# Performance work log

Measured on AMD Instinct MI355X. Metric: run time of the kernel, lower is better.

The kernel has to match this reference:

```python
import jax, jax.numpy as jnp
import numpy as np

S, D, H, L, FF = 4096, 128, 4, 3, 1024
DH = D // H
LN_EPS = 1e-5


def _layernorm(x, g, b):
    m = jnp.mean(x, axis=-1, keepdims=True)
    v = jnp.mean((x - m) ** 2, axis=-1, keepdims=True)
    return (x - m) * jax.lax.rsqrt(v + LN_EPS) * g + b


def setup_inputs() -> dict:
    key = jax.random.key(0)
    ks = jax.random.split(key, 16)
    w = lambda k, shp, s=0.05: jax.random.normal(k, shp, dtype=jnp.float32) * s
    return {
        "src": jax.random.normal(ks[0], (S, 1, D), dtype=jnp.float32),
        # per-layer transformer params, stacked on leading L axis
        "Wqkv": w(ks[1], (L, 3 * D, D)),
        "bqkv": jnp.zeros((L, 3 * D), jnp.float32),
        "Wo": w(ks[2], (L, D, D)),
        "bo": jnp.zeros((L, D), jnp.float32),
        "ln1_g": jnp.ones((L, D), jnp.float32),
        "ln1_b": jnp.zeros((L, D), jnp.float32),
        "W1": w(ks[3], (L, FF, D)),
        "b1": jnp.zeros((L, FF), jnp.float32),
        "W2": w(ks[4], (L, D, FF)),
        "b2": jnp.zeros((L, D), jnp.float32),
        "ln2_g": jnp.ones((L, D), jnp.float32),
        "ln2_b": jnp.zeros((L, D), jnp.float32),
        "fc1_W": w(ks[5], (D, D)),
        "fc1_b": jnp.zeros((D,), jnp.float32),
        "fc2_W": w(ks[6], (D, D)),
        "fc2_b": jnp.zeros((D,), jnp.float32),
    }


def reference(src, Wqkv, bqkv, Wo, bo, ln1_g, ln1_b, W1, b1, W2, b2,
              ln2_g, ln2_b, fc1_W, fc1_b, fc2_W, fc2_b):
    x = src[:, 0, :]  # [S, D] (batch=1, squeezed as in the torch module)
    scale = 1.0 / np.sqrt(DH).astype(np.float32)
    for l in range(L):  # small fixed layer count
        # --- self-attention (post-norm, as in torch TransformerEncoderLayer, eval mode) ---
        qkv = x @ Wqkv[l].T + bqkv[l]                      # [S, 3D]
        q, k, v = jnp.split(qkv, 3, axis=-1)
        q = q.reshape(S, H, DH)
        k = k.reshape(S, H, DH)
        v = v.reshape(S, H, DH)
        att = jax.nn.softmax(jnp.einsum('shd,thd->hst', q, k) * scale, axis=-1)
        o = jnp.einsum('hst,thd->shd', att, v).reshape(S, D)
        o = o @ Wo[l].T + bo[l]
        x = _layernorm(x + o, ln1_g[l], ln1_b[l])
        # --- feed-forward ---
        f = jax.nn.relu(x @ W1[l].T + b1[l]) @ W2[l].T + b2[l]
        x = _layernorm(x + f, ln2_g[l], ln2_b[l])
    # head
    x = jax.nn.relu(x @ fc1_W.T + fc1_b)
    x = x @ fc2_W.T + fc2_b
    # pairwise cosine similarity, clamped at min 1e-6 (vectorized form of pCosineSim)
    xn = x / jnp.linalg.norm(x, axis=1, keepdims=True)
    return jnp.maximum(xn @ xn.T, 1e-6)
```

## Files before the change

### kernel.cpp

```cpp
#include <hip/hip_runtime.h>
#include <math.h>

#define S 4096
#define QK_SCALE 0.17677669529663687f
#define LOG2E    1.44269504088896f
#define SPLIT 8
#define KS (S / SPLIT)

typedef _Float16 f16x8 __attribute__((ext_vector_type(8)));
typedef _Float16 f16x4 __attribute__((ext_vector_type(4)));
typedef _Float16 f16x2 __attribute__((ext_vector_type(2)));
typedef float f32x4 __attribute__((ext_vector_type(4)));

template<int R>
__device__ __forceinline__ void stageT(_Float16 (*dst)[136], const _Float16* __restrict__ src,
                                       int ld, int row0, int col0, int tid) {
    int r = tid >> 4, cb = (tid & 15) * 8;
#pragma unroll
    for (int v = 0; v < R / 16; v++)
        *(f16x8*)&dst[v * 16 + r][cb] =
            *(const f16x8*)(src + (size_t)(row0 + v * 16 + r) * ld + col0 + cb);
}

__device__ __forceinline__ void stageA_f16(_Float16 (*dst)[72], const _Float16* src,
                                           int ld, int row0, int col0, int tid) {
    int sr = tid >> 1, sc = (tid & 1) * 32;
    const _Float16* p = src + (size_t)(row0 + sr) * ld + col0 + sc;
#pragma unroll
    for (int v = 0; v < 4; v++)
        *(f16x8*)&dst[sr][sc + v * 8] = *(const f16x8*)(p + v * 8);
}

__device__ __forceinline__ void mfma_tiles(_Float16 (*Ah)[72], _Float16 (*Bh)[72],
                                           int wrow, int wcol, int lc, int lr,
                                           f32x4 acc[4][4]) {
#pragma unroll
    for (int ks = 0; ks < 2; ks++) {
        f16x8 afr[4], bfr[4];
#pragma unroll
        for (int t = 0; t < 4; t++) {
            afr[t] = *(const f16x8*)&Ah[wrow + t * 16 + lc][ks * 32 + lr * 8];
            bfr[t] = *(const f16x8*)&Bh[wcol + t * 16 + lc][ks * 32 + lr * 8];
        }
#pragma unroll
        for (int i = 0; i < 4; i++)
#pragma unroll
            for (int j = 0; j < 4; j++)
                acc[i][j] = __builtin_amdgcn_mfma_f32_16x16x32_f16(
                    afr[i], bfr[j], acc[i][j], 0, 0, 0);
    }
}

__global__ __launch_bounds__(256) void cvt_weights(const float* __restrict__ q,
                                                   const float* __restrict__ wo,
                                                   const float* __restrict__ w1,
                                                   const float* __restrict__ w2,
                                                   const float* __restrict__ f1,
                                                   const float* __restrict__ f2,
                                                   _Float16* __restrict__ dst)
{
    int bb = blockIdx.x;
    const float* src; size_t dof; int lb;
    if (bb < 144)      { src = q;  dof = 0;      lb = bb; }
    else if (bb < 192) { src = wo; dof = 147456; lb = bb - 144; }
    else if (bb < 576) { src = w1; dof = 196608; lb = bb - 192; }
    else if (bb < 960) { src = w2; dof = 589824; lb = bb - 576; }
    else if (bb < 976) { src = f1; dof = 983040; lb = bb - 960; }
    else               { src = f2; dof = 999424; lb = bb - 976; }
    int i = lb * 1024 + threadIdx.x * 4;
    float4 v = *(const float4*)(src + i);
    f16x4 h = {(_Float16)v.x, (_Float16)v.y, (_Float16)v.z, (_Float16)v.w};
    *(f16x4*)(dst + dof + i) = h;
}

__global__ __launch_bounds__(256) void copy_x(const float* __restrict__ a,
                                              float* __restrict__ x,
                                              _Float16* __restrict__ xh) {
    int i = blockIdx.x * 256 + threadIdx.x;
    float4 v = ((const float4*)a)[i];
    ((float4*)x)[i] = v;
    f16x4 h = {(_Float16)v.x, (_Float16)v.y, (_Float16)v.z, (_Float16)v.w};
    ((f16x4*)xh)[i] = h;
}

__global__ __launch_bounds__(256) void gemm_qkv(const _Float16* __restrict__ xh,
                                                const _Float16* __restrict__ Wh,
                                                const float* __restrict__ bias,
                                                _Float16* __restrict__ qh,
                                                _Float16* __restrict__ kh,
                                                _Float16* __restrict__ vt)
{
    __shared__ _Float16 Ah[32][136], Bh[128][136];
    int tid = threadIdx.x, w = tid >> 6, l = tid & 63, lc = l & 15, lr = l >> 4;
    int wr = w >> 1, wc = w & 1;
    int m0 = blockIdx.x * 32, by = blockIdx.y;

    stageT<32>(Ah, xh, 128, m0, 0, tid);
    stageT<128>(Bh, Wh, 128, by * 128, 0, tid);
    __syncthreads();

    f32x4 acc[4];
#pragma unroll
    for (int j = 0; j < 4; j++) acc[j] = {0.f, 0.f, 0.f, 0.f};
#pragma unroll
    for (int ks = 0; ks < 4; ks++) {
        f16x8 af = *(const f16x8*)&Ah[wr * 16 + lc][ks * 32 + lr * 8];
#pragma unroll
        for (int j = 0; j < 4; j++) {
            f16x8 bf = *(const f16x8*)&Bh[wc * 64 + j * 16 + lc][ks * 32 + lr * 8];
            acc[j] = __builtin_amdgcn_mfma_f32_16x16x32_f16(af, bf, acc[j], 0, 0, 0);
        }
    }

    int mb = m0 + wr * 16 + lr * 4;
#pragma unroll
    for (int j = 0; j < 4; j++) {
        int n = wc * 64 + j * 16 + lc;
        float bb = bias[by * 128 + n];
        if (by == 0) {
#pragma unroll
            for (int r = 0; r < 4; r++)
                qh[(size_t)(mb + r) * 128 + n] =
                    (_Float16)((acc[j][r] + bb) * (QK_SCALE * LOG2E));
        } else if (by == 1) {
            int hh = n >> 5, d = n & 31;
#pragma unroll
            for (int r = 0; r < 4; r++)
                kh[((size_t)hh * S + mb + r) * 32 + d] = (_Float16)(acc[j][r] + bb);
        } else {
            f16x4 pk;
#pragma unroll
            for (int r = 0; r < 4; r++) pk[r] = (_Float16)(acc[j][r] + bb);
            *(f16x4*)&vt[(size_t)n * S + mb] = pk;
        }
    }
}

__global__ __launch_bounds__(256) void attn_mfma(const _Float16* __restrict__ qh,
                                                 const _Float16* __restrict__ kh,
                                                 const _Float16* __restrict__ vt,
                                                 _Float16* __restrict__ part,
                                                 float* __restrict__ mll)
{
    __shared__ _Float16 Ks[64][48];
    __shared__ _Float16 Vt[32][72];
    __shared__ _Float16 Ps[4][16][72];
    int h = blockIdx.y, q0 = blockIdx.x * 64, z = blockIdx.z;
    int tid = threadIdx.x;
    int w = tid >> 6, l = tid & 63;
    int lc = l & 15, lr = l >> 4;

    f16x8 qf = *(const f16x8*)&qh[(size_t)(q0 + w * 16 + lc) * 128 + h * 32 + lr * 8];

    f32x4 o0 = {0.f, 0.f, 0.f, 0.f}, o1 = {0.f, 0.f, 0.f, 0.f};
    float lp[4] = {0.f, 0.f, 0.f, 0.f};

    const _Float16* khh = kh + (size_t)h * S * 32;
    const _Float16* vth = vt + (size_t)h * 32 * S;

    for (int k0 = z * KS; k0 < z * KS + KS; k0 += 64) {
        __syncthreads();
        {
            int row = tid >> 2, dg = (tid & 3) * 8;
            *(f16x8*)&Ks[row][dg] = *(const f16x8*)&khh[(size_t)(k0 + row) * 32 + dg];
            int dim = tid >> 3, kg = (tid & 7) * 8;
            *(f16x8*)&Vt[dim][kg] = *(const f16x8*)&vth[(size_t)dim * S + k0 + kg];
        }
        __syncthreads();

        f32x4 st[4];
#pragma unroll
        for (int t = 0; t < 4; t++) {
            f16x8 kf = *(const f16x8*)&Ks[t * 16 + lc][lr * 8];
            f32x4 zz = {0.f, 0.f, 0.f, 0.f};
            st[t] = __builtin_amdgcn_mfma_f32_16x16x32_f16(qf, kf, zz, 0, 0, 0);
        }

#pragma unroll
        for (int i = 0; i < 4; i++) {
            float p0 = exp2f(st[0][i]), p1 = exp2f(st[1][i]);
            float p2 = exp2f(st[2][i]), p3 = exp2f(st[3][i]);
            lp[i] += (p0 + p1) + (p2 + p3);
            Ps[w][lr * 4 + i][lc]      = (_Float16)p0;
            Ps[w][lr * 4 + i][16 + lc] = (_Float16)p1;
            Ps[w][lr * 4 + i][32 + lc] = (_Float16)p2;
            Ps[w][lr * 4 + i][48 + lc] = (_Float16)p3;
        }
        asm volatile("s_waitcnt lgkmcnt(0)" ::: "memory");
#pragma unroll
        for (int ch = 0; ch < 2; ch++) {
            f16x8 pf = *(const f16x8*)&Ps[w][lc][ch * 32 + lr * 8];
            f16x8 v0 = *(const f16x8*)&Vt[lc][ch * 32 + lr * 8];
            f16x8 v1 = *(const f16x8*)&Vt[16 + lc][ch * 32 + lr * 8];
            o0 = __builtin_amdgcn_mfma_f32_16x16x32_f16(pf, v0, o0, 0, 0, 0);
            o1 = __builtin_amdgcn_mfma_f32_16x16x32_f16(pf, v1, o1, 0, 0, 0);
        }
    }

#pragma unroll
    for (int i = 0; i < 4; i++) {
#pragma unroll
        for (int off = 1; off < 16; off <<= 1) lp[i] += __shfl_xor(lp[i], off);
    }

    _Float16* pz = part + (size_t)z * 524288;
#pragma unroll
    for (int i = 0; i < 4; i++) {
        int q = q0 + w * 16 + lr * 4 + i;
        pz[(size_t)q * 128 + h * 32 + lc]      = (_Float16)o0[i];
        pz[(size_t)q * 128 + h * 32 + 16 + lc] = (_Float16)o1[i];
        if (lc == 0) mll[((size_t)z * 4 + h) * 4096 + q] = lp[i];
    }
}

__global__ __launch_bounds__(256) void wo_ln_merge(const _Float16* __restrict__ part,
                                                   const float* __restrict__ mll,
                                                   const _Float16* __restrict__ Wh,
                                                   const float* __restrict__ bias,
                                                   float* __restrict__ x,
                                                   _Float16* __restrict__ xh,
                                                   const float* __restrict__ g,
                                                   const float* __restrict__ b)
{
    __shared__ _Float16 Ah[16][136], Bh[128][136];
    __shared__ float Red[16][4][2];
    int tid = threadIdx.x, w = tid >> 6, l = tid & 63, lc = l & 15, lr = l >> 4;
    int m0 = blockIdx.x * 16;

    {
        int row = tid >> 4, col0 = (tid & 15) * 8;
        int q = m0 + row, hh = col0 >> 5;
        float lsum = 0.f;
#pragma unroll
        for (int s = 0; s < SPLIT; s++) lsum += mll[((size_t)s * 4 + hh) * 4096 + q];
        float am[8];
#pragma unroll
        for (int e = 0; e < 8; e++) am[e] = 0.f;
#pragma unroll
        for (int s = 0; s < SPLIT; s++) {
            f16x8 t = *(const f16x8*)&part[(size_t)s * 524288 + (size_t)q * 128 + col0];
#pragma unroll
            for (int e = 0; e < 8; e++) am[e] += (float)t[e];
        }
        float inv = 1.f / lsum;
        f16x8 hv;
#pragma unroll
        for (int e = 0; e < 8; e++) hv[e] = (_Float16)(am[e] * inv);
        *(f16x8*)&Ah[row][col0] = hv;
    }
    stageT<128>(Bh, Wh, 128, 0, 0, tid);
    __syncthreads();

    f32x4 acc[2];
#pragma unroll
    for (int j = 0; j < 2; j++) acc[j] = {0.f, 0.f, 0.f, 0.f};
#pragma unroll
    for (int ks = 0; ks < 4; ks++) {
        f16x8 af = *(const f16x8*)&Ah[lc][ks * 32 + lr * 8];
#pragma unroll
        for (int j = 0; j < 2; j++) {
            f16x8 bf = *(const f16x8*)&Bh[w * 32 + j * 16 + lc][ks * 32 + lr * 8];
            acc[j] = __builtin_amdgcn_mfma_f32_16x16x32_f16(af, bf, acc[j], 0, 0, 0);
        }
    }

#pragma unroll
    for (int j = 0; j < 2; j++) {
        int n = w * 32 + j * 16 + lc;
        float bb = bias[n];
#pragma unroll
        for (int r = 0; r < 4; r++)
            acc[j][r] += bb + x[(size_t)(m0 + lr * 4 + r) * 128 + n];
    }
#pragma unroll
    for (int r = 0; r < 4; r++) {
        float s1 = acc[0][r] + acc[1][r];
        float s2 = acc[0][r] * acc[0][r] + acc[1][r] * acc[1][r];
#pragma unroll
        for (int off = 1; off < 16; off <<= 1) {
            s1 += __shfl_xor(s1, off);
            s2 += __shfl_xor(s2, off);
        }
        if (lc == 0) { Red[lr * 4 + r][w][0] = s1; Red[lr * 4 + r][w][1] = s2; }
    }
    __syncthreads();
#pragma unroll
    for (int r = 0; r < 4; r++) {
        int rl = lr * 4 + r;
        float S1 = (Red[rl][0][0] + Red[rl][1][0]) + (Red[rl][2][0] + Red[rl][3][0]);
        float S2 = (Red[rl][0][1] + Red[rl][1][1]) + (Red[rl][2][1] + Red[rl][3][1]);
        float mean = S1 * (1.0f / 128.0f);
        float var = S2 * (1.0f / 128.0f) - mean * mean;
        float inv = rsqrtf(var + 1e-5f);
        int m = m0 + rl;
#pragma unroll
        for (int j = 0; j < 2; j++) {
            int n = w * 32 + j * 16 + lc;
            float o = (acc[j][r] - mean) * inv * g[n] + b[n];
            x[(size_t)m * 128 + n] = o;
            xh[(size_t)m * 128 + n] = (_Float16)o;
        }
    }
}

__global__ __launch_bounds__(256) void ffn_pair(const _Float16* __restrict__ xh,
                                                const _Float16* __restrict__ W1h,
                                                const float* __restrict__ b1,
                                                const _Float16* __restrict__ W2h,
                                                _Float16* __restrict__ wpart)
{
    __shared__ _Float16 Ah[64][136], Bh[128][136];
    int tid = threadIdx.x, w = tid >> 6, l = tid & 63, lc = l & 15, lr = l >> 4;
    int wr = w >> 1, wc = w & 1;
    int m0 = blockIdx.x * 64, c = blockIdx.y;

    stageT<64>(Ah, xh, 128, m0, 0, tid);
    stageT<128>(Bh, W1h, 128, c * 128, 0, tid);
    __syncthreads();

    f32x4 acc[2][4];
#pragma unroll
    for (int i = 0; i < 2; i++)
#pragma unroll
        for (int j = 0; j < 4; j++) acc[i][j] = {0.f, 0.f, 0.f, 0.f};
#pragma unroll
    for (int ks = 0; ks < 4; ks++) {
        f16x8 af0 = *(const f16x8*)&Ah[wr * 32 + lc][ks * 32 + lr * 8];
        f16x8 af1 = *(const f16x8*)&Ah[wr * 32 + 16 + lc][ks * 32 + lr * 8];
#pragma unroll
        for (int j = 0; j < 4; j++) {
            f16x8 bf = *(const f16x8*)&Bh[wc * 64 + j * 16 + lc][ks * 32 + lr * 8];
            acc[0][j] = __builtin_amdgcn_mfma_f32_16x16x32_f16(af0, bf, acc[0][j], 0, 0, 0);
            acc[1][j] = __builtin_amdgcn_mfma_f32_16x16x32_f16(af1, bf, acc[1][j], 0, 0, 0);
        }
    }
    __syncthreads();

#pragma unroll
    for (int i = 0; i < 2; i++)
#pragma unroll
        for (int j = 0; j < 4; j++) {
            int n = wc * 64 + j * 16 + lc;
            float bb = b1[c * 128 + n];
#pragma unroll
            for (int r = 0; r < 4; r++)
                Ah[wr * 32 + i * 16 + lr * 4 + r][n] =
                    (_Float16)fmaxf(acc[i][j][r] + bb, 0.f);
        }
    stageT<128>(Bh, W2h, 1024, 0, c * 128, tid);
    __syncthreads();

    f32x4 oacc[2][4];
#pragma unroll
    for (int i = 0; i < 2; i++)
#pragma unroll
        for (int j = 0; j < 4; j++) oacc[i][j] = {0.f, 0.f, 0.f, 0.f};
#pragma unroll
    for (int ks = 0; ks < 4; ks++) {
        f16x8 af0 = *(const f16x8*)&Ah[wr * 32 + lc][ks * 32 + lr * 8];
        f16x8 af1 = *(const f16x8*)&Ah[wr * 32 + 16 + lc][ks * 32 + lr * 8];
#pragma unroll
        for (int j = 0; j < 4; j++) {
            f16x8 bf = *(const f16x8*)&Bh[wc * 64 + j * 16 + lc][ks * 32 + lr * 8];
            oacc[0][j] = __builtin_amdgcn_mfma_f32_16x16x32_f16(af0, bf, oacc[0][j], 0, 0, 0);
            oacc[1][j] = __builtin_amdgcn_mfma_f32_16x16x32_f16(af1, bf, oacc[1][j], 0, 0, 0);
        }
    }

    _Float16* pz = wpart + (size_t)c * 524288;
#pragma unroll
    for (int i = 0; i < 2; i++) {
        int mb = m0 + wr * 32 + i * 16 + lr * 4;
#pragma unroll
        for (int j = 0; j < 4; j++) {
            int n = wc * 64 + j * 16 + lc;
#pragma unroll
            for (int r = 0; r < 4; r++)
                pz[(size_t)(mb + r) * 128 + n] = (_Float16)oacc[i][j][r];
        }
    }
}

__global__ __launch_bounds__(256) void reduce8_ln(const _Float16* __restrict__ part,
                                                  const float* __restrict__ bias,
                                                  float* __restrict__ x,
                                                  _Float16* __restrict__ xh,
                                                  const float* __restrict__ g,
                                                  const float* __restrict__ b)
{
    int row  = blockIdx.x * 4 + (threadIdx.x >> 6);
    int lane = threadIdx.x & 63;
    size_t base = (size_t)row * 128;
    int c = lane * 2;
    float a0 = 0.f, a1 = 0.f;
#pragma unroll
    for (int s = 0; s < 8; s++) {
        f16x2 p = *(const f16x2*)&part[(size_t)s * 524288 + base + c];
        a0 += (float)p[0]; a1 += (float)p[1];
    }
    float2 bv = *(const float2*)&bias[c];
    float2 xv = *(const float2*)&x[base + c];
    a0 += bv.x + xv.x; a1 += bv.y + xv.y;
    float s = a0 + a1;
#pragma unroll
    for (int off = 32; off; off >>= 1) s += __shfl_xor(s, off);
    float mean = s * (1.0f / 128.0f);
    float d0 = a0 - mean, d1 = a1 - mean;
    float v = d0 * d0 + d1 * d1;
#pragma unroll
    for (int off = 32; off; off >>= 1) v += __shfl_xor(v, off);
    float inv = rsqrtf(v * (1.0f / 128.0f) + 1e-5f);
    float2 gv = *(const float2*)&g[c];
    float2 bb = *(const float2*)&b[c];
    float o0 = d0 * inv * gv.x + bb.x, o1 = d1 * inv * gv.y + bb.y;
    float2 r; r.x = o0; r.y = o1;
    *(float2*)&x[base + c] = r;
    f16x2 rh = {(_Float16)o0, (_Float16)o1};
    *(f16x2*)&xh[base + c] = rh;
}

__global__ __launch_bounds__(256) void fc_fused(const _Float16* __restrict__ xh,
                                                const _Float16* __restrict__ W1h,
                                                const float* __restrict__ b1f,
                                                const _Float16* __restrict__ W2h,
                                                const float* __restrict__ b2f,
                                                _Float16* __restrict__ aoh)
{
    __shared__ _Float16 Ah[16][136], Bh[128][136];
    __shared__ float Red[16][4];
    int tid = threadIdx.x, w = tid >> 6, l = tid & 63, lc = l & 15, lr = l >> 4;
    int m0 = blockIdx.x * 16;

    stageT<16>(Ah, xh, 128, m0, 0, tid);
    stageT<128>(Bh, W1h, 128, 0, 0, tid);
    __syncthreads();

    f32x4 acc[2];
#pragma unroll
    for (int j = 0; j < 2; j++) acc[j] = {0.f, 0.f, 0.f, 0.f};
#pragma unroll
    for (int ks = 0; ks < 4; ks++) {
        f16x8 af = *(const f16x8*)&Ah[lc][ks * 32 + lr * 8];
#pragma unroll
        for (int j = 0; j < 2; j++) {
            f16x8 bf = *(const f16x8*)&Bh[w * 32 + j * 16 + lc][ks * 32 + lr * 8];
            acc[j] = __builtin_amdgcn_mfma_f32_16x16x32_f16(af, bf, acc[j], 0, 0, 0);
        }
    }
    __syncthreads();
#pragma unroll
    for (int j = 0; j < 2; j++) {
        int n = w * 32 + j * 16 + lc;
        float bb = b1f[n];
#pragma unroll
        for (int r = 0; r < 4; r++)
            Ah[lr * 4 + r][n] = (_Float16)fmaxf(acc[j][r] + bb, 0.f);
    }
    stageT<128>(Bh, W2h, 128, 0, 0, tid);
    __syncthreads();

    f32x4 o[2];
#pragma unroll
    for (int j = 0; j < 2; j++) o[j] = {0.f, 0.f, 0.f, 0.f};
#pragma unroll
    for (int ks = 0; ks < 4; ks++) {
        f16x8 af = *(const f16x8*)&Ah[lc][ks * 32 + lr * 8];
#pragma unroll
        for (int j = 0; j < 2; j++) {
            f16x8 bf = *(const f16x8*)&Bh[w * 32 + j * 16 + lc][ks * 32 + lr * 8];
            o[j] = __builtin_amdgcn_mfma_f32_16x16x32_f16(af, bf, o[j], 0, 0, 0);
        }
    }
#pragma unroll
    for (int j = 0; j < 2; j++) {
        float bb = b2f[w * 32 + j * 16 + lc];
#pragma unroll
        for (int r = 0; r < 4; r++) o[j][r] += bb;
    }
#pragma unroll
    for (int r = 0; r < 4; r++) {
        float s2 = o[0][r] * o[0][r] + o[1][r] * o[1][r];
#pragma unroll
        for (int off = 1; off < 16; off <<= 1) s2 += __shfl_xor(s2, off);
        if (lc == 0) Red[lr * 4 + r][w] = s2;
    }
    __syncthreads();
#pragma unroll
    for (int r = 0; r < 4; r++) {
        int rl = lr * 4 + r;
        float inv = rsqrtf((Red[rl][0] + Red[rl][1]) + (Red[rl][2] + Red[rl][3]));
        int m = m0 + rl;
#pragma unroll
        for (int j = 0; j < 2; j++) {
            int n = w * 32 + j * 16 + lc;
            aoh[(size_t)m * 128 + n] = (_Float16)(o[j][r] * inv);
        }
    }
}

__global__ __launch_bounds__(256) void gram_f16(const _Float16* __restrict__ aoh,
                                                float* __restrict__ C)
{
    __shared__ _Float16 Ah[128][72], Bh[128][72];
    int tid = threadIdx.x, w = tid >> 6, l = tid & 63, lc = l & 15, lr = l >> 4;
    int wrow = (w >> 1) * 64, wcol = (w & 1) * 64;
    int m0 = blockIdx.x * 128, n0 = blockIdx.y * 128;

    f32x4 acc[4][4];
#pragma unroll
    for (int i = 0; i < 4; i++)
#pragma unroll
        for (int j = 0; j < 4; j++) acc[i][j] = {0.f, 0.f, 0.f, 0.f};

#pragma unroll
    for (int k0 = 0; k0 < 128; k0 += 64) {
        __syncthreads();
        stageA_f16(Ah, aoh, 128, m0, k0, tid);
        stageA_f16(Bh, aoh, 128, n0, k0, tid);
        __syncthreads();
        mfma_tiles(Ah, Bh, wrow, wcol, lc, lr, acc);
    }

#pragma unroll
    for (int i = 0; i < 4; i++) {
        int mb = m0 + wrow + i * 16 + lr * 4;
#pragma unroll
        for (int j = 0; j < 4; j++) {
            int n = n0 + wcol + j * 16 + lc;
#pragma unroll
            for (int r = 0; r < 4; r++)
                C[(size_t)(mb + r) * 4096 + n] = fmaxf(acc[i][j][r], 1e-6f);
        }
    }
}

extern "C" void kernel_launch(void* const* d_in, const int* in_sizes, int n_in,
                              void* d_out, int out_size, void* d_ws, size_t ws_size,
                              hipStream_t stream)
{
    const float* src  = (const float*)d_in[0];
    const float* Wqkv = (const float*)d_in[1];
    const float* bqkv = (const float*)d_in[2];
    const float* Wo   = (const float*)d_in[3];
    const float* bo   = (const float*)d_in[4];
    const float* ln1g = (const float*)d_in[5];
    const float* ln1b = (const float*)d_in[6];
    const float* W1   = (const float*)d_in[7];
    const float* b1   = (const float*)d_in[8];
    const float* W2   = (const float*)d_in[9];
    const float* b2   = (const float*)d_in[10];
    const float* ln2g = (const float*)d_in[11];
    const float* ln2b = (const float*)d_in[12];
    const float* fc1W = (const float*)d_in[13];
    const float* fc1b = (const float*)d_in[14];
    const float* fc2W = (const float*)d_in[15];
    const float* fc2b = (const float*)d_in[16];

    float* ws = (float*)d_ws;
    float*    x   = ws;
    _Float16* xh  = (_Float16*)(ws + 524288);
    _Float16* aoh = (_Float16*)(ws + 786432);
    _Float16* qh  = (_Float16*)(ws + 1048576);
    _Float16* kh  = (_Float16*)(ws + 1310720);
    _Float16* vt  = (_Float16*)(ws + 1572864);
    float*    mll = ws + 1835008;

    _Float16* wpart = (_Float16*)d_out + 4194304;
    _Float16* apart = (_Float16*)d_out + 12582912;
    _Float16* wh    = (_Float16*)d_out + 16777216;
    float*    out   = (float*)d_out;

    _Float16* qkvh = wh;
    _Float16* woh  = wh + 147456;
    _Float16* w1h  = wh + 196608;
    _Float16* w2h  = wh + 589824;
    _Float16* fc1h = wh + 983040;
    _Float16* fc2h = wh + 999424;

    cvt_weights<<<992, 256, 0, stream>>>(Wqkv, Wo, W1, W2, fc1W, fc2W, wh);
    copy_x<<<512, 256, 0, stream>>>(src, x, xh);
    for (int l = 0; l < 3; l++) {
        gemm_qkv<<<dim3(128, 3), 256, 0, stream>>>(xh, qkvh + l * 49152,
                                                   bqkv + l * 384, qh, kh, vt);
        attn_mfma<<<dim3(64, 4, SPLIT), 256, 0, stream>>>(qh, kh, vt, apart, mll);
        wo_ln_merge<<<256, 256, 0, stream>>>(apart, mll, woh + l * 16384, bo + l * 128,
                                             x, xh, ln1g + l * 128, ln1b + l * 128);
        ffn_pair<<<dim3(64, 8), 256, 0, stream>>>(xh, w1h + l * 131072, b1 + l * 1024,
                                                  w2h + l * 131072, wpart);
        reduce8_ln<<<1024, 256, 0, stream>>>(wpart, b2 + l * 128, x, xh,
                                             ln2g + l * 128, ln2b + l * 128);
    }
    fc_fused<<<256, 256, 0, stream>>>(xh, fc1h, fc1b, fc2h, fc2b, aoh);
    gram_f16<<<dim3(32, 32), 256, 0, stream>>>(aoh, out);
}
```

Before: 273.4 us.

## Fuse setup kernels, double-buffer attention K/V, retile QKV and gram GEMMs

Merges the weight-conversion and input-copy kernels into one launch. The attention kernel now double-buffers its K/V shared tiles with register prefetch, computes S transposed so probabilities are written as packed pairs, and reduces the row sum with fewer shuffles. The QKV GEMM uses 16-row tiles to launch more blocks. The gram kernel stages the full K=128 at once with 64x128 tiles for more blocks. Together these target launch overhead, load latency in attention, and low occupancy, at the cost of more LDS per block and smaller tiles with less reuse.

```diff
diff --git a/kernel.cpp b/kernel.cpp
--- a/kernel.cpp
+++ b/kernel.cpp
@@ -22,65 +22,37 @@
             *(const f16x8*)(src + (size_t)(row0 + v * 16 + r) * ld + col0 + cb);
 }
 
-__device__ __forceinline__ void stageA_f16(_Float16 (*dst)[72], const _Float16* src,
-                                           int ld, int row0, int col0, int tid) {
-    int sr = tid >> 1, sc = (tid & 1) * 32;
-    const _Float16* p = src + (size_t)(row0 + sr) * ld + col0 + sc;
-#pragma unroll
-    for (int v = 0; v < 4; v++)
-        *(f16x8*)&dst[sr][sc + v * 8] = *(const f16x8*)(p + v * 8);
-}
-
-__device__ __forceinline__ void mfma_tiles(_Float16 (*Ah)[72], _Float16 (*Bh)[72],
-                                           int wrow, int wcol, int lc, int lr,
-                                           f32x4 acc[4][4]) {
-#pragma unroll
-    for (int ks = 0; ks < 2; ks++) {
-        f16x8 afr[4], bfr[4];
-#pragma unroll
-        for (int t = 0; t < 4; t++) {
-            afr[t] = *(const f16x8*)&Ah[wrow + t * 16 + lc][ks * 32 + lr * 8];
-            bfr[t] = *(const f16x8*)&Bh[wcol + t * 16 + lc][ks * 32 + lr * 8];
-        }
-#pragma unroll
-        for (int i = 0; i < 4; i++)
-#pragma unroll
-            for (int j = 0; j < 4; j++)
-                acc[i][j] = __builtin_amdgcn_mfma_f32_16x16x32_f16(
-                    afr[i], bfr[j], acc[i][j], 0, 0, 0);
-    }
-}
-
-__global__ __launch_bounds__(256) void cvt_weights(const float* __restrict__ q,
-                                                   const float* __restrict__ wo,
-                                                   const float* __restrict__ w1,
-                                                   const float* __restrict__ w2,
-                                                   const float* __restrict__ f1,
-                                                   const float* __restrict__ f2,
-                                                   _Float16* __restrict__ dst)
+__global__ __launch_bounds__(256) void setup_cvt(const float* __restrict__ q,
+                                                 const float* __restrict__ wo,
+                                                 const float* __restrict__ w1,
+                                                 const float* __restrict__ w2,
+                                                 const float* __restrict__ f1,
+                                                 const float* __restrict__ f2,
+                                                 _Float16* __restrict__ dst,
+                                                 const float* __restrict__ a,
+                                                 float* __restrict__ x,
+                                                 _Float16* __restrict__ xh)
 {
     int bb = blockIdx.x;
-    const float* src; size_t dof; int lb;
-    if (bb < 144)      { src = q;  dof = 0;      lb = bb; }
-    else if (bb < 192) { src = wo; dof = 147456; lb = bb - 144; }
-    else if (bb < 576) { src = w1; dof = 196608; lb = bb - 192; }
-    else if (bb < 960) { src = w2; dof = 589824; lb = bb - 576; }
-    else if (bb < 976) { src = f1; dof = 983040; lb = bb - 960; }
-    else               { src = f2; dof = 999424; lb = bb - 976; }
-    int i = lb * 1024 + threadIdx.x * 4;
-    float4 v = *(const float4*)(src + i);
-    f16x4 h = {(_Float16)v.x, (_Float16)v.y, (_Float16)v.z, (_Float16)v.w};
-    *(f16x4*)(dst + dof + i) = h;
-}
-
-__global__ __launch_bounds__(256) void copy_x(const float* __restrict__ a,
-                                              float* __restrict__ x,
-                                              _Float16* __restrict__ xh) {
-    int i = blockIdx.x * 256 + threadIdx.x;
-    float4 v = ((const float4*)a)[i];
-    ((float4*)x)[i] = v;
-    f16x4 h = {(_Float16)v.x, (_Float16)v.y, (_Float16)v.z, (_Float16)v.w};
-    ((f16x4*)xh)[i] = h;
+    if (bb < 992) {
+        const float* src; size_t dof; int lb;
+        if (bb < 144)      { src = q;  dof = 0;      lb = bb; }
+        else if (bb < 192) { src = wo; dof = 147456; lb = bb - 144; }
+        else if (bb < 576) { src = w1; dof = 196608; lb = bb - 192; }
+        else if (bb < 960) { src = w2; dof = 589824; lb = bb - 576; }
+        else if (bb < 976) { src = f1; dof = 983040; lb = bb - 960; }
+        else               { src = f2; dof = 999424; lb = bb - 976; }
+        int i = lb * 1024 + threadIdx.x * 4;
+        float4 v = *(const float4*)(src + i);
+        f16x4 h = {(_Float16)v.x, (_Float16)v.y, (_Float16)v.z, (_Float16)v.w};
+        *(f16x4*)(dst + dof + i) = h;
+    } else {
+        int i = (bb - 992) * 256 + threadIdx.x;
+        float4 v = ((const float4*)a)[i];
+        ((float4*)x)[i] = v;
+        f16x4 h = {(_Float16)v.x, (_Float16)v.y, (_Float16)v.z, (_Float16)v.w};
+        ((f16x4*)xh)[i] = h;
+    }
 }
 
 __global__ __launch_bounds__(256) void gemm_qkv(const _Float16* __restrict__ xh,
@@ -90,32 +62,31 @@
                                                 _Float16* __restrict__ kh,
                                                 _Float16* __restrict__ vt)
 {
-    __shared__ _Float16 Ah[32][136], Bh[128][136];
+    __shared__ _Float16 Ah[16][136], Bh[128][136];
     int tid = threadIdx.x, w = tid >> 6, l = tid & 63, lc = l & 15, lr = l >> 4;
-    int wr = w >> 1, wc = w & 1;
-    int m0 = blockIdx.x * 32, by = blockIdx.y;
-
-    stageT<32>(Ah, xh, 128, m0, 0, tid);
+    int m0 = blockIdx.x * 16, by = blockIdx.y;
+
+    stageT<16>(Ah, xh, 128, m0, 0, tid);
     stageT<128>(Bh, Wh, 128, by * 128, 0, tid);
     __syncthreads();
 
-    f32x4 acc[4];
-#pragma unroll
-    for (int j = 0; j < 4; j++) acc[j] = {0.f, 0.f, 0.f, 0.f};
-#pragma unroll
-    for (int ks = 0; ks < 4; ks++) {
-        f16x8 af = *(const f16x8*)&Ah[wr * 16 + lc][ks * 32 + lr * 8];
-#pragma unroll
-        for (int j = 0; j < 4; j++) {
-            f16x8 bf = *(const f16x8*)&Bh[wc * 64 + j * 16 + lc][ks * 32 + lr * 8];
+    f32x4 acc[2];
+#pragma unroll
+    for (int j = 0; j < 2; j++) acc[j] = {0.f, 0.f, 0.f, 0.f};
+#pragma unroll
+    for (int ks = 0; ks < 4; ks++) {
+        f16x8 af = *(const f16x8*)&Ah[lc][ks * 32 + lr * 8];
+#pragma unroll
+        for (int j = 0; j < 2; j++) {
+            f16x8 bf = *(const f16x8*)&Bh[w * 32 + j * 16 + lc][ks * 32 + lr * 8];
             acc[j] = __builtin_amdgcn_mfma_f32_16x16x32_f16(af, bf, acc[j], 0, 0, 0);
         }
     }
 
-    int mb = m0 + wr * 16 + lr * 4;
-#pragma unroll
-    for (int j = 0; j < 4; j++) {
-        int n = wc * 64 + j * 16 + lc;
+    int mb = m0 + lr * 4;
+#pragma unroll
+    for (int j = 0; j < 2; j++) {
+        int n = w * 32 + j * 16 + lc;
         float bb = bias[by * 128 + n];
         if (by == 0) {
 #pragma unroll
@@ -142,8 +113,8 @@
                                                  _Float16* __restrict__ part,
                                                  float* __restrict__ mll)
 {
-    __shared__ _Float16 Ks[64][48];
-    __shared__ _Float16 Vt[32][72];
+    __shared__ _Float16 Ks[2][64][32];
+    __shared__ _Float16 Vt[2][32][72];
     __shared__ _Float16 Ps[4][16][72];
     int h = blockIdx.y, q0 = blockIdx.x * 64, z = blockIdx.z;
     int tid = threadIdx.x;
@@ -152,56 +123,71 @@
 
     f16x8 qf = *(const f16x8*)&qh[(size_t)(q0 + w * 16 + lc) * 128 + h * 32 + lr * 8];
 
-    f32x4 o0 = {0.f, 0.f, 0.f, 0.f}, o1 = {0.f, 0.f, 0.f, 0.f};
-    float lp[4] = {0.f, 0.f, 0.f, 0.f};
-
     const _Float16* khh = kh + (size_t)h * S * 32;
     const _Float16* vth = vt + (size_t)h * 32 * S;
 
-    for (int k0 = z * KS; k0 < z * KS + KS; k0 += 64) {
-        __syncthreads();
-        {
-            int row = tid >> 2, dg = (tid & 3) * 8;
-            *(f16x8*)&Ks[row][dg] = *(const f16x8*)&khh[(size_t)(k0 + row) * 32 + dg];
-            int dim = tid >> 3, kg = (tid & 7) * 8;
-            *(f16x8*)&Vt[dim][kg] = *(const f16x8*)&vth[(size_t)dim * S + k0 + kg];
-        }
-        __syncthreads();
+    int krow = tid >> 2, kcol = (tid & 3) * 8;
+    int vrow = tid >> 3, vcol = (tid & 7) * 8;
+
+    f32x4 o0 = {0.f, 0.f, 0.f, 0.f}, o1 = {0.f, 0.f, 0.f, 0.f};
+    float lp = 0.f;
+
+    int k0 = z * KS;
+    {
+        f16x8 kr = *(const f16x8*)&khh[(size_t)(k0 + krow) * 32 + kcol];
+        f16x8 vr = *(const f16x8*)&vth[(size_t)vrow * S + k0 + vcol];
+        *(f16x8*)&Ks[0][krow][kcol] = kr;
+        *(f16x8*)&Vt[0][vrow][vcol] = vr;
+    }
+    __syncthreads();
+
+    int cur = 0;
+#pragma unroll 1
+    for (int t8 = 0; t8 < KS / 64; t8++) {
+        bool more = (t8 + 1 < KS / 64);
+        f16x8 kr, vr;
+        if (more) {
+            int kn = k0 + (t8 + 1) * 64;
+            kr = *(const f16x8*)&khh[(size_t)(kn + krow) * 32 + kcol];
+            vr = *(const f16x8*)&vth[(size_t)vrow * S + kn + vcol];
+        }
 
         f32x4 st[4];
 #pragma unroll
         for (int t = 0; t < 4; t++) {
-            f16x8 kf = *(const f16x8*)&Ks[t * 16 + lc][lr * 8];
+            f16x8 kf = *(const f16x8*)&Ks[cur][t * 16 + lc][lr * 8];
             f32x4 zz = {0.f, 0.f, 0.f, 0.f};
-            st[t] = __builtin_amdgcn_mfma_f32_16x16x32_f16(qf, kf, zz, 0, 0, 0);
-        }
-
-#pragma unroll
-        for (int i = 0; i < 4; i++) {
-            float p0 = exp2f(st[0][i]), p1 = exp2f(st[1][i]);
-            float p2 = exp2f(st[2][i]), p3 = exp2f(st[3][i]);
-            lp[i] += (p0 + p1) + (p2 + p3);
-            Ps[w][lr * 4 + i][lc]      = (_Float16)p0;
-            Ps[w][lr * 4 + i][16 + lc] = (_Float16)p1;
-            Ps[w][lr * 4 + i][32 + lc] = (_Float16)p2;
-            Ps[w][lr * 4 + i][48 + lc] = (_Float16)p3;
+            st[t] = __builtin_amdgcn_mfma_f32_16x16x32_f16(kf, qf, zz, 0, 0, 0);
+        }
+#pragma unroll
+        for (int t = 0; t < 4; t++) {
+            float p0 = exp2f(st[t][0]), p1 = exp2f(st[t][1]);
+            float p2 = exp2f(st[t][2]), p3 = exp2f(st[t][3]);
+            lp += (p0 + p1) + (p2 + p3);
+            f16x2 h0 = {(_Float16)p0, (_Float16)p1};
+            f16x2 h1 = {(_Float16)p2, (_Float16)p3};
+            *(f16x2*)&Ps[w][lc][t * 16 + lr * 4]     = h0;
+            *(f16x2*)&Ps[w][lc][t * 16 + lr * 4 + 2] = h1;
         }
         asm volatile("s_waitcnt lgkmcnt(0)" ::: "memory");
 #pragma unroll
         for (int ch = 0; ch < 2; ch++) {
             f16x8 pf = *(const f16x8*)&Ps[w][lc][ch * 32 + lr * 8];
-            f16x8 v0 = *(const f16x8*)&Vt[lc][ch * 32 + lr * 8];
-            f16x8 v1 = *(const f16x8*)&Vt[16 + lc][ch * 32 + lr * 8];
+            f16x8 v0 = *(const f16x8*)&Vt[cur][lc][ch * 32 + lr * 8];
+            f16x8 v1 = *(const f16x8*)&Vt[cur][16 + lc][ch * 32 + lr * 8];
             o0 = __builtin_amdgcn_mfma_f32_16x16x32_f16(pf, v0, o0, 0, 0, 0);
             o1 = __builtin_amdgcn_mfma_f32_16x16x32_f16(pf, v1, o1, 0, 0, 0);
         }
-    }
-
-#pragma unroll
-    for (int i = 0; i < 4; i++) {
-#pragma unroll
-        for (int off = 1; off < 16; off <<= 1) lp[i] += __shfl_xor(lp[i], off);
-    }
+        if (more) {
+            *(f16x8*)&Ks[cur ^ 1][krow][kcol] = kr;
+            *(f16x8*)&Vt[cur ^ 1][vrow][vcol] = vr;
+            __syncthreads();
+        }
+        cur ^= 1;
+    }
+
+    lp += __shfl_xor(lp, 16);
+    lp += __shfl_xor(lp, 32);
 
     _Float16* pz = part + (size_t)z * 524288;
 #pragma unroll
@@ -209,8 +195,8 @@
         int q = q0 + w * 16 + lr * 4 + i;
         pz[(size_t)q * 128 + h * 32 + lc]      = (_Float16)o0[i];
         pz[(size_t)q * 128 + h * 32 + 16 + lc] = (_Float16)o1[i];
-        if (lc == 0) mll[((size_t)z * 4 + h) * 4096 + q] = lp[i];
-    }
+    }
+    if (l < 16) mll[((size_t)z * 4 + h) * 4096 + q0 + w * 16 + lc] = lp;
 }
 
 __global__ __launch_bounds__(256) void wo_ln_merge(const _Float16* __restrict__ part,
@@ -501,32 +487,38 @@
 __global__ __launch_bounds__(256) void gram_f16(const _Float16* __restrict__ aoh,
                                                 float* __restrict__ C)
 {
-    __shared__ _Float16 Ah[128][72], Bh[128][72];
+    __shared__ _Float16 Ah[64][136], Bh[128][136];
     int tid = threadIdx.x, w = tid >> 6, l = tid & 63, lc = l & 15, lr = l >> 4;
-    int wrow = (w >> 1) * 64, wcol = (w & 1) * 64;
-    int m0 = blockIdx.x * 128, n0 = blockIdx.y * 128;
-
-    f32x4 acc[4][4];
-#pragma unroll
-    for (int i = 0; i < 4; i++)
+    int wr = w >> 1, wc = w & 1;
+    int m0 = blockIdx.x * 64, n0 = blockIdx.y * 128;
+
+    stageT<64>(Ah, aoh, 128, m0, 0, tid);
+    stageT<128>(Bh, aoh, 128, n0, 0, tid);
+    __syncthreads();
+
+    f32x4 acc[2][4];
+#pragma unroll
+    for (int i = 0; i < 2; i++)
 #pragma unroll
         for (int j = 0; j < 4; j++) acc[i][j] = {0.f, 0.f, 0.f, 0.f};
-
-#pragma unroll
-    for (int k0 = 0; k0 < 128; k0 += 64) {
-        __syncthreads();
-        stageA_f16(Ah, aoh, 128, m0, k0, tid);
-        stageA_f16(Bh, aoh, 128, n0, k0, tid);
-        __syncthreads();
-        mfma_tiles(Ah, Bh, wrow, wcol, lc, lr, acc);
-    }
-
-#pragma unroll
-    for (int i = 0; i < 4; i++) {
-        int mb = m0 + wrow + i * 16 + lr * 4;
+#pragma unroll
+    for (int ks = 0; ks < 4; ks++) {
+        f16x8 af0 = *(const f16x8*)&Ah[wr * 32 + lc][ks * 32 + lr * 8];
+        f16x8 af1 = *(const f16x8*)&Ah[wr * 32 + 16 + lc][ks * 32 + lr * 8];
 #pragma unroll
         for (int j = 0; j < 4; j++) {
-            int n = n0 + wcol + j * 16 + lc;
+            f16x8 bf = *(const f16x8*)&Bh[wc * 64 + j * 16 + lc][ks * 32 + lr * 8];
+            acc[0][j] = __builtin_amdgcn_mfma_f32_16x16x32_f16(af0, bf, acc[0][j], 0, 0, 0);
+            acc[1][j] = __builtin_amdgcn_mfma_f32_16x16x32_f16(af1, bf, acc[1][j], 0, 0, 0);
+        }
+    }
+
+#pragma unroll
+    for (int i = 0; i < 2; i++) {
+        int mb = m0 + wr * 32 + i * 16 + lr * 4;
+#pragma unroll
+        for (int j = 0; j < 4; j++) {
+            int n = n0 + wc * 64 + j * 16 + lc;
 #pragma unroll
             for (int r = 0; r < 4; r++)
                 C[(size_t)(mb + r) * 4096 + n] = fmaxf(acc[i][j][r], 1e-6f);
@@ -577,10 +569,10 @@
     _Float16* fc1h = wh + 983040;
     _Float16* fc2h = wh + 999424;
 
-    cvt_weights<<<992, 256, 0, stream>>>(Wqkv, Wo, W1, W2, fc1W, fc2W, wh);
-    copy_x<<<512, 256, 0, stream>>>(src, x, xh);
+    setup_cvt<<<1504, 256, 0, stream>>>(Wqkv, Wo, W1, W2, fc1W, fc2W, wh,
+                                        src, x, xh);
     for (int l = 0; l < 3; l++) {
-        gemm_qkv<<<dim3(128, 3), 256, 0, stream>>>(xh, qkvh + l * 49152,
+        gemm_qkv<<<dim3(256, 3), 256, 0, stream>>>(xh, qkvh + l * 49152,
                                                    bqkv + l * 384, qh, kh, vt);
         attn_mfma<<<dim3(64, 4, SPLIT), 256, 0, stream>>>(qh, kh, vt, apart, mll);
         wo_ln_merge<<<256, 256, 0, stream>>>(apart, mll, woh + l * 16384, bo + l * 128,
@@ -591,5 +583,5 @@
                                              ln2g + l * 128, ln2b + l * 128);
     }
     fc_fused<<<256, 256, 0, stream>>>(xh, fc1h, fc1b, fc2h, fc2b, aoh);
-    gram_f16<<<dim3(32, 32), 256, 0, stream>>>(aoh, out);
-}
+    gram_f16<<<dim3(64, 32), 256, 0, stream>>>(aoh, out);
+}
```

After: 263.3 us. -3.7%, faster.
